# Kernel tuning notes

Measured on AMD Instinct MI355X. Metric: run time of the kernel, lower is better.

The kernel has to match this reference:

```python
import jax, jax.numpy as jnp
import numpy as np

OW = 80                # cfg.out_size[1]
POS_THRESHOLD = 0.005  # cfg.pos_threshold
LN_EPS = 1e-5


def setup_inputs() -> dict:
    key = jax.random.key(0)
    ks = jax.random.split(key, 6)
    B, C, T, N = 16, 1024, 64, 12
    NFG = NFR = NFG_ONE = 1024
    s = 0.02
    return {
        "x": jax.random.normal(ks[0], (B, C, T, N), dtype=jnp.float32),
        "A": jax.random.uniform(ks[1], (B, T, N, 4), dtype=jnp.float32),
        "w_theta": jax.random.normal(ks[2], (NFG, NFR), dtype=jnp.float32) * s,
        "b_theta": jnp.zeros((NFR,), dtype=jnp.float32),
        "w_phi": jax.random.normal(ks[3], (NFG, NFR), dtype=jnp.float32) * s,
        "b_phi": jnp.zeros((NFR,), dtype=jnp.float32),
        "w_gcn": jax.random.normal(ks[4], (NFG, NFG_ONE), dtype=jnp.float32) * s,
        "ln_w": jnp.ones((N, NFG_ONE), dtype=jnp.float32),
        "ln_b": jnp.zeros((N, NFG_ONE), dtype=jnp.float32),
    }


def reference(x, A, w_theta, b_theta, w_phi, b_phi, w_gcn, ln_w, ln_b):
    B, C, T, N = x.shape
    # box centers -> pairwise euclidean distances per (B*T) frame
    boxes = A.reshape(-1, 4)
    cx = (boxes[:, 0] + boxes[:, 2]) * 0.5
    cy = (boxes[:, 1] + boxes[:, 3]) * 0.5
    pos = jnp.stack([cx, cy], axis=-1).reshape(B * T, N, 2)
    sq = jnp.sum(pos * pos, axis=2)  # [BT, N]
    d2 = sq[:, :, None] - 2.0 * jnp.einsum('bnc,bmc->bnm', pos, pos) + sq[:, None, :]
    dist = jnp.sqrt(jnp.maximum(d2, 0.0))  # clamp tiny negatives from fp error
    position_mask = dist > POS_THRESHOLD * OW  # [BT, N, N]

    # features: [B, C, T, N] -> [BT, N, C]
    feat = jnp.transpose(x, (0, 2, 3, 1)).reshape(B * T, N, C)
    theta = feat @ w_theta + b_theta  # [BT, N, NFR]
    phi = feat @ w_phi + b_phi        # [BT, N, NFR]
    scale = 1.0 / jnp.sqrt(jnp.asarray(theta.shape[-1], dtype=feat.dtype))
    logits = jnp.einsum('bnf,bmf->bnm', theta, phi) * scale
    logits = jnp.where(position_mask, -jnp.inf, logits)
    relation_graph = jax.nn.softmax(logits, axis=2)  # [BT, N, N]

    # graph conv: aggregate then project (no bias)
    agg = jnp.einsum('bnm,bmc->bnc', relation_graph, feat) @ w_gcn  # [BT, N, NFG_ONE]

    # LayerNorm over the last two dims [N, NFG_ONE]
    mu = jnp.mean(agg, axis=(1, 2), keepdims=True)
    var = jnp.var(agg, axis=(1, 2), keepdims=True)
    normed = (agg - mu) / jnp.sqrt(var + LN_EPS) * ln_w + ln_b
    out = jax.nn.relu(normed)
    return out, relation_graph
```

## Files before the change

kernel.cpp:

```cpp
#include <hip/hip_runtime.h>
#include <math.h>
#include <stdint.h>

#define NDIM   12
#define KDIM   1024
#define BT_TOT 1024
#define M_TOT  (BT_TOT * NDIM)
#define OUT_MAIN (M_TOT * KDIM)
#define MASK_TH 0.4f
#define LN_EPS 1e-5f

typedef float f32x4 __attribute__((ext_vector_type(4)));
typedef short bf16x8 __attribute__((ext_vector_type(8)));
typedef short bf16x4 __attribute__((ext_vector_type(4)));

__device__ __forceinline__ float bf2f(unsigned short u) {
    return __uint_as_float(((unsigned int)u) << 16);
}
__device__ __forceinline__ unsigned short f2bf(float f) {
    unsigned int u = __float_as_uint(f);
    return (unsigned short)((u + 0x7FFFu + ((u >> 16) & 1u)) >> 16);
}
__device__ __forceinline__ void gld16(const void* g, void* l) {
    __builtin_amdgcn_global_load_lds(
        (const __attribute__((address_space(1))) unsigned int*)g,
        (__attribute__((address_space(3))) unsigned int*)l, 16, 0, 0);
}

__global__ __launch_bounds__(256)
void prep_kernel(const float* __restrict__ x,   const float* __restrict__ wth,
                 const float* __restrict__ wph, const float* __restrict__ bth,
                 const float* __restrict__ wg,
                 unsigned short* __restrict__ wgT, float* __restrict__ vbuf,
                 unsigned short* __restrict__ featB, unsigned short* __restrict__ MtB)
{
    const int bid = blockIdx.x, tid = threadIdx.x;
    __shared__ __align__(16) char ldsb[16384];

    if (bid < 64) {
        const int m0 = (bid >> 3) * 128, n0 = (bid & 7) * 128;
        const int lane = tid & 63, wid = tid >> 6;
        const int wr = wid >> 1, wc = wid & 1;
        unsigned short* As = (unsigned short*)ldsb;
        unsigned short* Bs = As + 4096;
        f32x4 acc[4][4] = {};
        const int row = tid >> 1, half = tid & 1;

        for (int k0 = 0; k0 < KDIM; k0 += 32) {
            const float* ga = wph + (size_t)(m0 + row) * KDIM + k0 + half * 16;
            const float* gb = wth + (size_t)(n0 + row) * KDIM + k0 + half * 16;
            unsigned short pa[16], pb[16];
            #pragma unroll
            for (int j = 0; j < 4; ++j) {
                const float4 va = ((const float4*)ga)[j];
                const float4 vb = ((const float4*)gb)[j];
                pa[j*4+0] = f2bf(va.x); pa[j*4+1] = f2bf(va.y);
                pa[j*4+2] = f2bf(va.z); pa[j*4+3] = f2bf(va.w);
                pb[j*4+0] = f2bf(vb.x); pb[j*4+1] = f2bf(vb.y);
                pb[j*4+2] = f2bf(vb.z); pb[j*4+3] = f2bf(vb.w);
            }
            const int le = row * 32 + half * 16;
            *(uint4*)&As[le]     = ((const uint4*)pa)[0];
            *(uint4*)&As[le + 8] = ((const uint4*)pa)[1];
            *(uint4*)&Bs[le]     = ((const uint4*)pb)[0];
            *(uint4*)&Bs[le + 8] = ((const uint4*)pb)[1];
            __syncthreads();

            bf16x8 af[4], bfr[4];
            const int rA = wr * 64 + (lane & 15);
            const int rB = wc * 64 + (lane & 15);
            const int kq = (lane >> 4) * 8;
            #pragma unroll
            for (int mi = 0; mi < 4; ++mi)
                af[mi] = *(const bf16x8*)&As[(rA + mi * 16) * 32 + kq];
            #pragma unroll
            for (int ni = 0; ni < 4; ++ni)
                bfr[ni] = *(const bf16x8*)&Bs[(rB + ni * 16) * 32 + kq];
            #pragma unroll
            for (int mi = 0; mi < 4; ++mi)
                #pragma unroll
                for (int ni = 0; ni < 4; ++ni)
                    acc[mi][ni] = __builtin_amdgcn_mfma_f32_16x16x32_bf16(
                        af[mi], bfr[ni], acc[mi][ni], 0, 0, 0);
            __syncthreads();
        }
        #pragma unroll
        for (int mi = 0; mi < 4; ++mi) {
            const int gr0 = m0 + wr * 64 + mi * 16 + ((tid & 63) >> 4) * 4;
            #pragma unroll
            for (int ni = 0; ni < 4; ++ni) {
                const int gc = n0 + wc * 64 + ni * 16 + (tid & 15);
                const f32x4 v = acc[mi][ni];
                #pragma unroll
                for (int reg = 0; reg < 4; ++reg)
                    MtB[(size_t)(gr0 + reg) * KDIM + gc] = f2bf(v[reg]);
            }
        }
    } else if (bid < 6208) {
        float (*tileF)[33] = (float(*)[33])ldsb;
        const int b4 = bid - 64;
        const int px = b4 % 24;
        const int rest = b4 / 24;
        const int cx = rest & 15, b = rest >> 4;
        const int p0 = px * 32, c0 = cx * 64;
        const float* src = x + (size_t)b * KDIM * 768;
        #pragma unroll
        for (int i = 0; i < 8; ++i) {
            const int cl = (tid >> 5) + i * 8;
            tileF[cl][tid & 31] = src[(size_t)(c0 + cl) * 768 + p0 + (tid & 31)];
        }
        __syncthreads();
        unsigned short* dst = featB + ((size_t)b * 768 + p0) * KDIM;
        #pragma unroll
        for (int i = 0; i < 8; ++i) {
            const int pp = (tid >> 6) + i * 4;
            const int cl = tid & 63;
            dst[(size_t)pp * KDIM + c0 + cl] = f2bf(tileF[cl][pp]);
        }
    } else if (bid < 7232) {
        float (*tileF)[33] = (float(*)[33])ldsb;
        const int b2 = bid - 6208;
        const int o0 = (b2 & 31) * 32, c0 = (b2 >> 5) * 32;
        const int tx = tid & 31, ty = tid >> 5;
        #pragma unroll
        for (int i = 0; i < 4; ++i) {
            const int r = ty + i * 8;
            tileF[r][tx] = wg[(size_t)(c0 + r) * KDIM + o0 + tx];
        }
        __syncthreads();
        #pragma unroll
        for (int i = 0; i < 4; ++i) {
            const int r = ty + i * 8;
            wgT[(size_t)(o0 + r) * KDIM + c0 + tx] = f2bf(tileF[tx][r]);
        }
    } else {
        const int b3 = bid - 7232;
        const int lane = tid & 63, w = tid >> 6;
        const int j = b3 * 4 + w;
        const float4* row = (const float4*)(wph + (size_t)j * KDIM);
        const float4* bt4 = (const float4*)bth;
        float s = 0.f;
        #pragma unroll
        for (int i = 0; i < 4; ++i) {
            const float4 a = row[lane + i * 64], b = bt4[lane + i * 64];
            s += a.x * b.x + a.y * b.y + a.z * b.z + a.w * b.w;
        }
        #pragma unroll
        for (int msk = 32; msk >= 1; msk >>= 1) s += __shfl_xor(s, msk, 64);
        if (lane == 0) vbuf[j] = s;
    }
}

__global__ __launch_bounds__(256)
void gemm_kernel(const unsigned short* __restrict__ A,
                 const unsigned short* __restrict__ B0, const unsigned short* __restrict__ B1,
                 unsigned short* __restrict__ C0, unsigned short* __restrict__ C1)
{
    const int bid = blockIdx.x;
    const int c = bid & 7, s = bid >> 3;
    const int n = s & 7, mm = (s >> 3) % 12, z = s / 96;
    const int m0 = (c * 12 + mm) * 128, n0 = n * 128;
    const unsigned short* B = z ? B1 : B0;
    unsigned short* C       = z ? C1 : C0;

    const int tid = threadIdx.x, lane = tid & 63, wid = tid >> 6;
    const int wr = wid >> 1, wc = wid & 1;

    __shared__ __align__(16) unsigned short As[128 * 64];
    __shared__ __align__(16) unsigned short Bs[128 * 64];

    f32x4 acc[4][4] = {};

    const int srow_w = wid * 8 + (lane >> 3);
    const int schunk = lane & 7;

    for (int k0 = 0; k0 < KDIM; k0 += 64) {
        #pragma unroll
        for (int i = 0; i < 4; ++i) {
            const int row = srow_w + i * 32;
            const int gchunk = schunk ^ (row & 7);
            const char* srcA = (const char*)A + ((size_t)(m0 + row) * KDIM + k0) * 2 + gchunk * 16;
            const char* srcB = (const char*)B + ((size_t)(n0 + row) * KDIM + k0) * 2 + gchunk * 16;
            char* la = (char*)As + i * 4096 + wid * 1024;
            char* lb = (char*)Bs + i * 4096 + wid * 1024;
            gld16(srcA, la);
            gld16(srcB, lb);
        }
        __syncthreads();

        #pragma unroll
        for (int ks = 0; ks < 2; ++ks) {
            bf16x8 af[4], bfr[4];
            const int cch = ks * 4 + (lane >> 4);
            #pragma unroll
            for (int mi = 0; mi < 4; ++mi) {
                const int r = wr * 64 + (lane & 15) + mi * 16;
                af[mi] = *(const bf16x8*)((const char*)As + r * 128 + ((cch ^ (r & 7)) * 16));
            }
            #pragma unroll
            for (int ni = 0; ni < 4; ++ni) {
                const int r = wc * 64 + (lane & 15) + ni * 16;
                bfr[ni] = *(const bf16x8*)((const char*)Bs + r * 128 + ((cch ^ (r & 7)) * 16));
            }
            #pragma unroll
            for (int mi = 0; mi < 4; ++mi)
                #pragma unroll
                for (int ni = 0; ni < 4; ++ni)
                    acc[mi][ni] = __builtin_amdgcn_mfma_f32_16x16x32_bf16(
                        af[mi], bfr[ni], acc[mi][ni], 0, 0, 0);
        }
        __syncthreads();
    }

    #pragma unroll
    for (int mi = 0; mi < 4; ++mi) {
        const int gr0 = m0 + wr * 64 + mi * 16 + (lane >> 4) * 4;
        #pragma unroll
        for (int ni = 0; ni < 4; ++ni) {
            const int gc = n0 + wc * 64 + ni * 16 + (lane & 15);
            const f32x4 v = acc[mi][ni];
            #pragma unroll
            for (int reg = 0; reg < 4; ++reg)
                C[(size_t)(gr0 + reg) * KDIM + gc] = f2bf(v[reg]);
        }
    }
}

__global__ __launch_bounds__(256)
void relf_kernel(const unsigned short* __restrict__ G,
                 const unsigned short* __restrict__ featB,
                 const unsigned short* __restrict__ H,
                 const float* __restrict__ Abox, const float* __restrict__ vbuf,
                 const float* __restrict__ lnw, const float* __restrict__ lnb,
                 float* __restrict__ out)
{
    const int bid = blockIdx.x;
    const int f = ((bid & 7) << 7) + (bid >> 3);
    const int tid = threadIdx.x, lane = tid & 63, w = tid >> 6;
    __shared__ float Lred[4][16][16];
    __shared__ float relS[12][12];
    __shared__ float cxS[12], cyS[12], sqS[12];
    __shared__ float qred[4][12];
    __shared__ float rs[2][256];

    if (tid < 12) {
        const float4 box = *(const float4*)(Abox + ((size_t)f * 12 + tid) * 4);
        const float cx = (box.x + box.z) * 0.5f, cy = (box.y + box.w) * 0.5f;
        cxS[tid] = cx; cyS[tid] = cy; sqS[tid] = cx * cx + cy * cy;
    }

    const int r = lane & 15, rr = r < 12 ? r : 0;
    const int kq = (lane >> 4) * 8;
    const unsigned short* gG = G + (size_t)(f * 12 + rr) * KDIM;
    const unsigned short* gF = featB + (size_t)(f * 12 + rr) * KDIM;
    f32x4 acc = {};
    float qp = 0.f;
    #pragma unroll
    for (int s8 = 0; s8 < 8; ++s8) {
        const int k0 = (w * 8 + s8) * 32 + kq;
        const bf16x8 a = *(const bf16x8*)(gG + k0);
        const bf16x8 b = *(const bf16x8*)(gF + k0);
        acc = __builtin_amdgcn_mfma_f32_16x16x32_bf16(a, b, acc, 0, 0, 0);
        const float4 v0 = *(const float4*)(vbuf + k0);
        const float4 v1 = *(const float4*)(vbuf + k0 + 4);
        qp += bf2f((unsigned short)b[0]) * v0.x + bf2f((unsigned short)b[1]) * v0.y
            + bf2f((unsigned short)b[2]) * v0.z + bf2f((unsigned short)b[3]) * v0.w
            + bf2f((unsigned short)b[4]) * v1.x + bf2f((unsigned short)b[5]) * v1.y
            + bf2f((unsigned short)b[6]) * v1.z + bf2f((unsigned short)b[7]) * v1.w;
    }
    qp += __shfl_xor(qp, 16, 64);
    qp += __shfl_xor(qp, 32, 64);
    if (lane < 12) qred[w][lane] = qp;
    {
        const int row0 = (lane >> 4) * 4, col = lane & 15;
        #pragma unroll
        for (int reg = 0; reg < 4; ++reg) Lred[w][row0 + reg][col] = acc[reg];
    }
    __syncthreads();

    if (tid < 12) {
        const int n = tid;
        float l[12], mx = -3.4e38f;
        #pragma unroll
        for (int m = 0; m < 12; ++m) {
            const float L = Lred[0][n][m] + Lred[1][n][m] + Lred[2][n][m] + Lred[3][n][m];
            const float qm = qred[0][m] + qred[1][m] + qred[2][m] + qred[3][m];
            float val = (L + qm) * 0.03125f;
            const float d2 = sqS[n] - 2.f * (cxS[n] * cxS[m] + cyS[n] * cyS[m]) + sqS[m];
            const float dist = sqrtf(fmaxf(d2, 0.f));
            if (dist > MASK_TH) val = -INFINITY;
            l[m] = val; mx = fmaxf(mx, val);
        }
        float s = 0.f, e[12];
        #pragma unroll
        for (int m = 0; m < 12; ++m) { e[m] = expf(l[m] - mx); s += e[m]; }
        const float inv = 1.f / s;
        float* orel = out + (size_t)OUT_MAIN + (size_t)f * 144 + n * 12;
        #pragma unroll
        for (int m = 0; m < 12; ++m) {
            const float rv = e[m] * inv;
            relS[n][m] = rv;
            orel[m] = rv;
        }
    }
    __syncthreads();

    const int c0 = tid * 4;
    float h[12][4];
    #pragma unroll
    for (int m = 0; m < 12; ++m) {
        const bf16x4 h4 = *(const bf16x4*)(H + (size_t)(f * 12 + m) * KDIM + c0);
        #pragma unroll
        for (int j = 0; j < 4; ++j) h[m][j] = bf2f((unsigned short)h4[j]);
    }
    float a2[12][4];
    float s = 0.f, s2 = 0.f;
    #pragma unroll
    for (int n = 0; n < 12; ++n) {
        float rn[12];
        #pragma unroll
        for (int m = 0; m < 12; ++m) rn[m] = relS[n][m];
        #pragma unroll
        for (int j = 0; j < 4; ++j) {
            float a = 0.f;
            #pragma unroll
            for (int m = 0; m < 12; ++m) a = fmaf(rn[m], h[m][j], a);
            a2[n][j] = a; s += a; s2 += a * a;
        }
    }
    rs[0][tid] = s; rs[1][tid] = s2;
    __syncthreads();
    for (int o = 128; o > 0; o >>= 1) {
        if (tid < o) { rs[0][tid] += rs[0][tid + o]; rs[1][tid] += rs[1][tid + o]; }
        __syncthreads();
    }
    const float mu = rs[0][0] * (1.f / 12288.f);
    const float var = rs[1][0] * (1.f / 12288.f) - mu * mu;
    const float rstd = rsqrtf(var + LN_EPS);

    #pragma unroll
    for (int n = 0; n < 12; ++n) {
        const float4 wv = *(const float4*)(lnw + (size_t)n * KDIM + c0);
        const float4 bv = *(const float4*)(lnb + (size_t)n * KDIM + c0);
        float4 ov;
        ov.x = fmaxf(fmaf((a2[n][0] - mu) * rstd, wv.x, bv.x), 0.f);
        ov.y = fmaxf(fmaf((a2[n][1] - mu) * rstd, wv.y, bv.y), 0.f);
        ov.z = fmaxf(fmaf((a2[n][2] - mu) * rstd, wv.z, bv.z), 0.f);
        ov.w = fmaxf(fmaf((a2[n][3] - mu) * rstd, wv.w, bv.w), 0.f);
        *(float4*)(out + (size_t)(f * 12 + n) * KDIM + c0) = ov;
    }
}

extern "C" void kernel_launch(void* const* d_in, const int* in_sizes, int n_in,
                              void* d_out, int out_size, void* d_ws, size_t ws_size,
                              hipStream_t stream) {
    const float* x   = (const float*)d_in[0];
    const float* A   = (const float*)d_in[1];
    const float* wth = (const float*)d_in[2];
    const float* bth = (const float*)d_in[3];
    const float* wph = (const float*)d_in[4];
    const float* wg  = (const float*)d_in[6];
    const float* lnw = (const float*)d_in[7];
    const float* lnb = (const float*)d_in[8];
    float* out = (float*)d_out;

    char* ws = (char*)d_ws;
    const size_t MB = 1ull << 20;
    unsigned short* featB = (unsigned short*)(ws);
    unsigned short* G     = (unsigned short*)(ws + 24 * MB);
    unsigned short* H     = (unsigned short*)(ws + 48 * MB);
    unsigned short* wgT   = (unsigned short*)(ws + 72 * MB);
    unsigned short* MtB   = (unsigned short*)(ws + 74 * MB);
    float* vbuf = (float*)(ws + 76 * MB);

    prep_kernel<<<7488, 256, 0, stream>>>(x, wth, wph, bth, wg,
                                          wgT, vbuf, featB, MtB);
    gemm_kernel<<<1536, 256, 0, stream>>>(featB, MtB, wgT, G, H);
    relf_kernel<<<BT_TOT, 256, 0, stream>>>(G, featB, H, A, vbuf, lnw, lnb, out);
}
```

Measured before the change: 226.3 us.

## Enlarge x transpose tiles with vectorized stores, use shuffle LayerNorm reduction

The x-to-bf16 transpose in prep_kernel now uses 64x64 tiles with 8-byte vectorized stores of four bf16 values instead of 32x64 tiles with scalar 2-byte stores. This cuts the block count and should improve write coalescing. The transpose blocks move to the end of the grid so the GEMM and weight-transpose blocks are scheduled first. In relf_kernel the 256-entry shared-memory tree reduction for the LayerNorm statistics becomes a wavefront shuffle reduction plus a 4-entry combine, removing many syncthreads, and the block-to-frame swizzle is dropped.

```diff
diff --git a/kernel.cpp b/kernel.cpp
--- a/kernel.cpp
+++ b/kernel.cpp
@@ -35,11 +35,12 @@
                  unsigned short* __restrict__ featB, unsigned short* __restrict__ MtB)
 {
     const int bid = blockIdx.x, tid = threadIdx.x;
-    __shared__ __align__(16) char ldsb[16384];
+    const int lane = tid & 63;
+    __shared__ __align__(16) char ldsb[17408];
 
     if (bid < 64) {
         const int m0 = (bid >> 3) * 128, n0 = (bid & 7) * 128;
-        const int lane = tid & 63, wid = tid >> 6;
+        const int wid = tid >> 6;
         const int wr = wid >> 1, wc = wid & 1;
         unsigned short* As = (unsigned short*)ldsb;
         unsigned short* Bs = As + 4096;
@@ -86,40 +87,19 @@
         }
         #pragma unroll
         for (int mi = 0; mi < 4; ++mi) {
-            const int gr0 = m0 + wr * 64 + mi * 16 + ((tid & 63) >> 4) * 4;
+            const int gr0 = m0 + wr * 64 + mi * 16 + (lane >> 4) * 4;
             #pragma unroll
             for (int ni = 0; ni < 4; ++ni) {
-                const int gc = n0 + wc * 64 + ni * 16 + (tid & 15);
+                const int gc = n0 + wc * 64 + ni * 16 + (lane & 15);
                 const f32x4 v = acc[mi][ni];
                 #pragma unroll
                 for (int reg = 0; reg < 4; ++reg)
                     MtB[(size_t)(gr0 + reg) * KDIM + gc] = f2bf(v[reg]);
             }
         }
-    } else if (bid < 6208) {
+    } else if (bid < 1088) {
         float (*tileF)[33] = (float(*)[33])ldsb;
-        const int b4 = bid - 64;
-        const int px = b4 % 24;
-        const int rest = b4 / 24;
-        const int cx = rest & 15, b = rest >> 4;
-        const int p0 = px * 32, c0 = cx * 64;
-        const float* src = x + (size_t)b * KDIM * 768;
-        #pragma unroll
-        for (int i = 0; i < 8; ++i) {
-            const int cl = (tid >> 5) + i * 8;
-            tileF[cl][tid & 31] = src[(size_t)(c0 + cl) * 768 + p0 + (tid & 31)];
-        }
-        __syncthreads();
-        unsigned short* dst = featB + ((size_t)b * 768 + p0) * KDIM;
-        #pragma unroll
-        for (int i = 0; i < 8; ++i) {
-            const int pp = (tid >> 6) + i * 4;
-            const int cl = tid & 63;
-            dst[(size_t)pp * KDIM + c0 + cl] = f2bf(tileF[cl][pp]);
-        }
-    } else if (bid < 7232) {
-        float (*tileF)[33] = (float(*)[33])ldsb;
-        const int b2 = bid - 6208;
+        const int b2 = bid - 64;
         const int o0 = (b2 & 31) * 32, c0 = (b2 >> 5) * 32;
         const int tx = tid & 31, ty = tid >> 5;
         #pragma unroll
@@ -133,9 +113,9 @@
             const int r = ty + i * 8;
             wgT[(size_t)(o0 + r) * KDIM + c0 + tx] = f2bf(tileF[tx][r]);
         }
-    } else {
-        const int b3 = bid - 7232;
-        const int lane = tid & 63, w = tid >> 6;
+    } else if (bid < 1344) {
+        const int b3 = bid - 1088;
+        const int w = tid >> 6;
         const int j = b3 * 4 + w;
         const float4* row = (const float4*)(wph + (size_t)j * KDIM);
         const float4* bt4 = (const float4*)bth;
@@ -148,6 +128,30 @@
         #pragma unroll
         for (int msk = 32; msk >= 1; msk >>= 1) s += __shfl_xor(s, msk, 64);
         if (lane == 0) vbuf[j] = s;
+    } else {
+        float (*tf)[66] = (float(*)[66])ldsb;
+        const int b4 = bid - 1344;
+        const int pt = b4 % 12;
+        const int rest = b4 / 12;
+        const int ct = rest & 15, b = rest >> 4;
+        const int p0 = pt * 64, c0 = ct * 64;
+        const float* src = x + (size_t)b * KDIM * 768;
+        #pragma unroll
+        for (int i = 0; i < 16; ++i) {
+            const int cl = (tid >> 6) + i * 4;
+            tf[cl][lane] = src[(size_t)(c0 + cl) * 768 + p0 + lane];
+        }
+        __syncthreads();
+        unsigned short* dstb = featB + ((size_t)b * 768 + p0) * KDIM + c0;
+        #pragma unroll
+        for (int pp = 0; pp < 4; ++pp) {
+            const int p = (tid >> 4) + pp * 16;
+            const int cc = (tid & 15) * 4;
+            unsigned short o4[4];
+            #pragma unroll
+            for (int k = 0; k < 4; ++k) o4[k] = f2bf(tf[cc + k][p]);
+            *(uint2*)(dstb + (size_t)p * KDIM + cc) = *(const uint2*)o4;
+        }
     }
 }
 
@@ -234,14 +238,13 @@
                  const float* __restrict__ lnw, const float* __restrict__ lnb,
                  float* __restrict__ out)
 {
-    const int bid = blockIdx.x;
-    const int f = ((bid & 7) << 7) + (bid >> 3);
+    const int f = blockIdx.x;
     const int tid = threadIdx.x, lane = tid & 63, w = tid >> 6;
     __shared__ float Lred[4][16][16];
     __shared__ float relS[12][12];
     __shared__ float cxS[12], cyS[12], sqS[12];
     __shared__ float qred[4][12];
-    __shared__ float rs[2][256];
+    __shared__ float rs[2][4];
 
     if (tid < 12) {
         const float4 box = *(const float4*)(Abox + ((size_t)f * 12 + tid) * 4);
@@ -328,14 +331,17 @@
             a2[n][j] = a; s += a; s2 += a * a;
         }
     }
-    rs[0][tid] = s; rs[1][tid] = s2;
+    #pragma unroll
+    for (int msk = 32; msk >= 1; msk >>= 1) {
+        s  += __shfl_xor(s,  msk, 64);
+        s2 += __shfl_xor(s2, msk, 64);
+    }
+    if (lane == 0) { rs[0][w] = s; rs[1][w] = s2; }
     __syncthreads();
-    for (int o = 128; o > 0; o >>= 1) {
-        if (tid < o) { rs[0][tid] += rs[0][tid + o]; rs[1][tid] += rs[1][tid + o]; }
-        __syncthreads();
-    }
-    const float mu = rs[0][0] * (1.f / 12288.f);
-    const float var = rs[1][0] * (1.f / 12288.f) - mu * mu;
+    const float S  = rs[0][0] + rs[0][1] + rs[0][2] + rs[0][3];
+    const float S2 = rs[1][0] + rs[1][1] + rs[1][2] + rs[1][3];
+    const float mu = S * (1.f / 12288.f);
+    const float var = S2 * (1.f / 12288.f) - mu * mu;
     const float rstd = rsqrtf(var + LN_EPS);
 
     #pragma unroll
@@ -373,7 +379,7 @@
     unsigned short* MtB   = (unsigned short*)(ws + 74 * MB);
     float* vbuf = (float*)(ws + 76 * MB);
 
-    prep_kernel<<<7488, 256, 0, stream>>>(x, wth, wph, bth, wg,
+    prep_kernel<<<4416, 256, 0, stream>>>(x, wth, wph, bth, wg,
                                           wgT, vbuf, featB, MtB);
     gemm_kernel<<<1536, 256, 0, stream>>>(featB, MtB, wgT, G, H);
     relf_kernel<<<BT_TOT, 256, 0, stream>>>(G, featB, H, A, vbuf, lnw, lnb, out);
```

Measured after the change: 231.7 us. +2.4%, slower.
